# Kernel optimization log

Measured on AMD Instinct MI355X. Metric: run time of the kernel, lower is better.

The kernel has to match this reference:

```python
import jax, jax.numpy as jnp
import numpy as np

NUM_GRAPHS = 512


def setup_inputs() -> dict:
    key = jax.random.key(0)
    ks = jax.random.split(key, 12)
    N, F = 100000, 9
    E = 1600000
    x = jax.random.normal(ks[0], (N, F), dtype=jnp.float32)
    edge_index = jax.random.randint(ks[1], (2, E), 0, N, dtype=jnp.int64)
    batch = jnp.sort(jax.random.randint(ks[2], (N,), 0, NUM_GRAPHS, dtype=jnp.int64))
    def lin(k, fan_in, fan_out):
        k1, k2 = jax.random.split(k)
        bound = 1.0 / np.sqrt(fan_in)
        W = jax.random.uniform(k1, (fan_out, fan_in), jnp.float32, -bound, bound)
        b = jax.random.uniform(k2, (fan_out,), jnp.float32, -bound, bound)
        return W, b
    W1, b1 = lin(ks[3], F, 64)
    W2, b2 = lin(ks[4], 64, 128)
    W3, b3 = lin(ks[5], 128, 64)
    Wfc, bfc = lin(ks[6], 64, 11)
    return {"x": x, "edge_index": edge_index, "batch": batch,
            "W1": W1, "b1": b1, "W2": W2, "b2": b2,
            "W3": W3, "b3": b3, "Wfc": Wfc, "bfc": bfc}


def reference(x, edge_index, batch, W1, b1, W2, b2, W3, b3, Wfc, bfc):
    N = x.shape[0]
    src, dst = edge_index[0], edge_index[1]

    def gin_layer(h, W, b):
        # GINConv (eps=0): Lin((1+eps)*h_i + sum_{j->i} h_j), then relu
        agg = jax.ops.segment_sum(h[src], dst, num_segments=N)
        return jax.nn.relu((h + agg) @ W.T + b)

    h = gin_layer(x, W1, b1)   # [N, 64]
    h = gin_layer(h, W2, b2)   # [N, 128]
    h = gin_layer(h, W3, b3)   # [N, 64]

    # global_mean_pool over graph ids
    sums = jax.ops.segment_sum(h, batch, num_segments=NUM_GRAPHS)           # [G, 64]
    counts = jax.ops.segment_sum(jnp.ones((N,), h.dtype), batch,
                                 num_segments=NUM_GRAPHS)                   # [G]
    pooled = sums / jnp.maximum(counts, 1.0)[:, None]
    return pooled @ Wfc.T + bfc  # [G, num_classes]
```

## Files before the change

kernel.cpp:

```cpp
#include <hip/hip_runtime.h>
#include <hip/hip_bf16.h>


#define NBLK 256
#define CFBS 512
#define RB   128
#define NBMAX 1024
#define SCBS 1024

__device__ inline float bf2f(unsigned short u) {
    return __uint_as_float((unsigned)u << 16);
}
__device__ inline unsigned short f2bf(float f) {
    unsigned x = __float_as_uint(f);
    return (unsigned short)((x + 0x7FFFu + ((x >> 16) & 1u)) >> 16);
}
__device__ inline float lo16(unsigned u) { return __uint_as_float(u << 16); }
__device__ inline float hi16(unsigned u) { return __uint_as_float(u & 0xFFFF0000u); }


__global__ __launch_bounds__(CFBS) void count_kernel(
    const int* __restrict__ dst, int* __restrict__ cnt, int E, int NB)
{
    __shared__ int hist[NBMAX];
    int tid = threadIdx.x;
    for (int i = tid; i < NBMAX; i += CFBS) hist[i] = 0;
    __syncthreads();
    for (int e = blockIdx.x * CFBS + tid; e < E; e += NBLK * CFBS)
        atomicAdd(&hist[dst[e] >> 7], 1);
    __syncthreads();
    for (int b = tid; b < NB; b += CFBS)
        cnt[b * NBLK + blockIdx.x] = hist[b];
}

__global__ __launch_bounds__(SCBS) void scan_k1(
    const int* __restrict__ cnt, int* __restrict__ ofs,
    int* __restrict__ part, int NT)
{
    __shared__ int tmp[SCBS];
    int i = blockIdx.x * SCBS + threadIdx.x;
    int v = (i < NT) ? cnt[i] : 0;
    tmp[threadIdx.x] = v;
    __syncthreads();
    for (int off = 1; off < SCBS; off <<= 1) {
        int t = (threadIdx.x >= off) ? tmp[threadIdx.x - off] : 0;
        __syncthreads();
        tmp[threadIdx.x] += t;
        __syncthreads();
    }
    if (i < NT) ofs[i] = tmp[threadIdx.x] - v;
    if (threadIdx.x == SCBS - 1) part[blockIdx.x] = tmp[threadIdx.x];
}

__global__ __launch_bounds__(SCBS) void scan_k2(int* __restrict__ part, int B)
{
    __shared__ int tmp[SCBS];
    int v = (threadIdx.x < B) ? part[threadIdx.x] : 0;
    tmp[threadIdx.x] = v;
    __syncthreads();
    for (int off = 1; off < SCBS; off <<= 1) {
        int t = (threadIdx.x >= off) ? tmp[threadIdx.x - off] : 0;
        __syncthreads();
        tmp[threadIdx.x] += t;
        __syncthreads();
    }
    if (threadIdx.x < B) part[threadIdx.x] = tmp[threadIdx.x] - v;
}

__global__ __launch_bounds__(SCBS) void scan_k3(
    int* __restrict__ ofs, const int* __restrict__ part, int NT)
{
    int i = blockIdx.x * SCBS + threadIdx.x;
    if (i < NT) ofs[i] += part[blockIdx.x];
}

__global__ __launch_bounds__(CFBS) void fillp_kernel(
    const int* __restrict__ src, const int* __restrict__ dst,
    const int* __restrict__ ofs, int* __restrict__ pairs, int E, int NB)
{
    __shared__ int cur[NBMAX];
    int tid = threadIdx.x;
    for (int b = tid; b < NB; b += CFBS)
        cur[b] = ofs[b * NBLK + blockIdx.x];
    __syncthreads();
    for (int e = blockIdx.x * CFBS + tid; e < E; e += NBLK * CFBS) {
        int d = dst[e];
        int b = d >> 7, dl = d & 127;
        int pos = atomicAdd(&cur[b], 1);
        pairs[pos] = (dl << 20) | src[e];
    }
}

__global__ __launch_bounds__(512) void bucket_csr_kernel(
    const int* __restrict__ pairs, const int* __restrict__ ofs,
    int* __restrict__ rowstart, int* __restrict__ eidx, int N, int E, int NB)
{
    __shared__ int deg[RB], pfx[RB], cur[RB];
    int tid = threadIdx.x;
    int b = blockIdx.x, n0 = b << 7;
    int e0 = ofs[b * NBLK];
    int e1 = (b + 1 < NB) ? ofs[(b + 1) * NBLK] : E;
    if (tid < RB) deg[tid] = 0;
    __syncthreads();
    for (int e = e0 + tid; e < e1; e += 512)
        atomicAdd(&deg[pairs[e] >> 20], 1);
    __syncthreads();
    if (tid < RB) pfx[tid] = deg[tid];
    __syncthreads();
    for (int off = 1; off < RB; off <<= 1) {
        int t = (tid < RB && tid >= off) ? pfx[tid - off] : 0;
        __syncthreads();
        if (tid < RB) pfx[tid] += t;
        __syncthreads();
    }
    if (tid < RB) {
        int ex = pfx[tid] - deg[tid];
        cur[tid] = ex;
        int n = n0 + tid;
        if (n < N) rowstart[n] = e0 + ex;
    }
    if (b == NB - 1 && tid == 0) rowstart[N] = E;
    __syncthreads();
    for (int e = e0 + tid; e < e1; e += 512) {
        int p = pairs[e];
        int pos = e0 + atomicAdd(&cur[p >> 20], 1);
        eidx[pos] = p & 0xFFFFF;
    }
}


__global__ __launch_bounds__(256) void xprep_kernel(
    const float* __restrict__ x, unsigned short* __restrict__ xb, int N)
{
    int n = blockIdx.x * 256 + threadIdx.x;
    if (n >= N) return;
    unsigned short r[16];
    #pragma unroll
    for (int k = 0; k < 9; ++k) r[k] = f2bf(x[(size_t)n * 9 + k]);
    #pragma unroll
    for (int k = 9; k < 16; ++k) r[k] = 0;
    uint4 u0, u1;
    u0.x = r[0] | ((unsigned)r[1] << 16);  u0.y = r[2] | ((unsigned)r[3] << 16);
    u0.z = r[4] | ((unsigned)r[5] << 16);  u0.w = r[6] | ((unsigned)r[7] << 16);
    u1.x = r[8] | ((unsigned)r[9] << 16);  u1.y = 0; u1.z = 0; u1.w = 0;
    *(uint4*)&xb[(size_t)n * 16]     = u0;
    *(uint4*)&xb[(size_t)n * 16 + 8] = u1;
}


__global__ __launch_bounds__(256) void node1v_kernel(
    const unsigned short* __restrict__ xb, const int* __restrict__ rs,
    const int* __restrict__ eidx, const float* __restrict__ W1,
    const float* __restrict__ b1, unsigned short* __restrict__ h1, int N)
{
    __shared__ float Wl[576];
    __shared__ float bl[64];
    for (int i = threadIdx.x; i < 576; i += 256) Wl[i] = W1[i];
    if (threadIdx.x < 64) bl[threadIdx.x] = b1[threadIdx.x];
    __syncthreads();
    int wid = threadIdx.x >> 6;
    int lane = threadIdx.x & 63;
    int g  = lane >> 2;
    int d4 = lane & 3;
    int nb = blockIdx.x * 16 + wid * 4;
    if (nb >= N) return;

    int n[4], e0[4], dg[4];
    float A0[4], A1[4], A2[4], A3[4];
    #pragma unroll
    for (int i = 0; i < 4; ++i) {
        n[i] = min(nb + i, N - 1);
        e0[i] = rs[n[i]];
        dg[i] = rs[n[i] + 1] - e0[i];
        A0[i] = A1[i] = A2[i] = A3[i] = 0.f;
    }
    #pragma unroll
    for (int i = 0; i < 4; ++i) {
        if (g == 0) {
            uint2 u = *(const uint2*)&xb[(size_t)n[i] * 16 + d4 * 4];
            A0[i] += lo16(u.x); A1[i] += hi16(u.x);
            A2[i] += lo16(u.y); A3[i] += hi16(u.y);
        }
    }
    int mdeg = max(max(dg[0], dg[1]), max(dg[2], dg[3]));
    for (int w0 = 0; w0 < mdeg; w0 += 64) {
        int sidx[4], wd[4];
        #pragma unroll
        for (int i = 0; i < 4; ++i) {
            wd[i] = min(max(dg[i] - w0, 0), 64);
            sidx[i] = (lane < wd[i]) ? eidx[e0[i] + w0 + lane] : 0;
        }
        int mwd = max(max(wd[0], wd[1]), max(wd[2], wd[3]));
        for (int c = 0; c < mwd; c += 16) {
            #pragma unroll
            for (int i = 0; i < 4; ++i) {
                int idx = c + g;
                int s = __shfl(sidx[i], idx < wd[i] ? idx : 0);
                float m = (idx < wd[i]) ? 1.f : 0.f;
                uint2 u = *(const uint2*)&xb[(size_t)s * 16 + d4 * 4];
                A0[i] += m * lo16(u.x); A1[i] += m * hi16(u.x);
                A2[i] += m * lo16(u.y); A3[i] += m * hi16(u.y);
            }
        }
    }
    #pragma unroll
    for (int m = 4; m < 64; m <<= 1) {
        #pragma unroll
        for (int i = 0; i < 4; ++i) {
            A0[i] += __shfl_xor(A0[i], m); A1[i] += __shfl_xor(A1[i], m);
            A2[i] += __shfl_xor(A2[i], m); A3[i] += __shfl_xor(A3[i], m);
        }
    }
    const float* wr = &Wl[lane * 9];
    #pragma unroll
    for (int i = 0; i < 4; ++i) {
        float xv0 = __shfl(A0[i], 0), xv1 = __shfl(A1[i], 0);
        float xv2 = __shfl(A2[i], 0), xv3 = __shfl(A3[i], 0);
        float xv4 = __shfl(A0[i], 1), xv5 = __shfl(A1[i], 1);
        float xv6 = __shfl(A2[i], 1), xv7 = __shfl(A3[i], 1);
        float xv8 = __shfl(A0[i], 2);
        float s = bl[lane] + xv0 * wr[0] + xv1 * wr[1] + xv2 * wr[2]
                + xv3 * wr[3] + xv4 * wr[4] + xv5 * wr[5] + xv6 * wr[6]
                + xv7 * wr[7] + xv8 * wr[8];
        if (nb + i < N)
            h1[(size_t)(nb + i) * 64 + lane] = f2bf(fmaxf(s, 0.f));
    }
}


template<bool BIAS_RELU>
__global__ __launch_bounds__(256) void gather64v_kernel(
    const unsigned short* __restrict__ feat, const int* __restrict__ rs,
    const int* __restrict__ eidx, const float* __restrict__ bias,
    unsigned short* __restrict__ out, int N)
{
    int wid = threadIdx.x >> 6;
    int lane = threadIdx.x & 63;
    int g  = lane >> 4;
    int d4 = lane & 15;
    int nb = blockIdx.x * 16 + wid * 4;
    if (nb >= N) return;

    int n[4], e0[4], dg[4];
    float A0[4], A1[4], A2[4], A3[4];
    #pragma unroll
    for (int i = 0; i < 4; ++i) {
        n[i] = min(nb + i, N - 1);
        e0[i] = rs[n[i]];
        dg[i] = rs[n[i] + 1] - e0[i];
        A0[i] = A1[i] = A2[i] = A3[i] = 0.f;
    }
    #pragma unroll
    for (int i = 0; i < 4; ++i) {
        if (g == 0) {
            uint2 u = *(const uint2*)&feat[(size_t)n[i] * 64 + d4 * 4];
            A0[i] += lo16(u.x); A1[i] += hi16(u.x);
            A2[i] += lo16(u.y); A3[i] += hi16(u.y);
        }
    }
    int mdeg = max(max(dg[0], dg[1]), max(dg[2], dg[3]));
    for (int w0 = 0; w0 < mdeg; w0 += 64) {
        int sidx[4], wd[4];
        #pragma unroll
        for (int i = 0; i < 4; ++i) {
            wd[i] = min(max(dg[i] - w0, 0), 64);
            sidx[i] = (lane < wd[i]) ? eidx[e0[i] + w0 + lane] : 0;
        }
        int mwd = max(max(wd[0], wd[1]), max(wd[2], wd[3]));
        for (int c = 0; c < mwd; c += 16) {
            #pragma unroll
            for (int i = 0; i < 4; ++i) {
                int i0 = c + g, i1 = c + 4 + g;
                int i2 = c + 8 + g, i3 = c + 12 + g;
                int s0 = __shfl(sidx[i], i0 < wd[i] ? i0 : 0);
                int s1 = __shfl(sidx[i], i1 < wd[i] ? i1 : 0);
                int s2 = __shfl(sidx[i], i2 < wd[i] ? i2 : 0);
                int s3 = __shfl(sidx[i], i3 < wd[i] ? i3 : 0);
                float m0 = (i0 < wd[i]) ? 1.f : 0.f;
                float m1 = (i1 < wd[i]) ? 1.f : 0.f;
                float m2 = (i2 < wd[i]) ? 1.f : 0.f;
                float m3 = (i3 < wd[i]) ? 1.f : 0.f;
                uint2 u0 = *(const uint2*)&feat[(size_t)s0 * 64 + d4 * 4];
                uint2 u1 = *(const uint2*)&feat[(size_t)s1 * 64 + d4 * 4];
                uint2 u2 = *(const uint2*)&feat[(size_t)s2 * 64 + d4 * 4];
                uint2 u3 = *(const uint2*)&feat[(size_t)s3 * 64 + d4 * 4];
                A0[i] += (m0 * lo16(u0.x) + m1 * lo16(u1.x))
                       + (m2 * lo16(u2.x) + m3 * lo16(u3.x));
                A1[i] += (m0 * hi16(u0.x) + m1 * hi16(u1.x))
                       + (m2 * hi16(u2.x) + m3 * hi16(u3.x));
                A2[i] += (m0 * lo16(u0.y) + m1 * lo16(u1.y))
                       + (m2 * lo16(u2.y) + m3 * lo16(u3.y));
                A3[i] += (m0 * hi16(u0.y) + m1 * hi16(u1.y))
                       + (m2 * hi16(u2.y) + m3 * hi16(u3.y));
            }
        }
    }
    #pragma unroll
    for (int m = 16; m < 64; m <<= 1) {
        #pragma unroll
        for (int i = 0; i < 4; ++i) {
            A0[i] += __shfl_xor(A0[i], m); A1[i] += __shfl_xor(A1[i], m);
            A2[i] += __shfl_xor(A2[i], m); A3[i] += __shfl_xor(A3[i], m);
        }
    }
    float4 bv = make_float4(0.f, 0.f, 0.f, 0.f);
    if (BIAS_RELU) bv = *(const float4*)&bias[d4 * 4];
    #pragma unroll
    for (int i = 0; i < 4; ++i) {
        if (g == 0 && nb + i < N) {
            float a0 = A0[i], a1 = A1[i], a2 = A2[i], a3 = A3[i];
            if (BIAS_RELU) {
                a0 = fmaxf(a0 + bv.x, 0.f); a1 = fmaxf(a1 + bv.y, 0.f);
                a2 = fmaxf(a2 + bv.z, 0.f); a3 = fmaxf(a3 + bv.w, 0.f);
            }
            ushort4 u;
            u.x = f2bf(a0); u.y = f2bf(a1); u.z = f2bf(a2); u.w = f2bf(a3);
            *(ushort4*)&out[(size_t)(nb + i) * 64 + d4 * 4] = u;
        }
    }
}


__global__ __launch_bounds__(256) void linear23_fused_kernel(
    const unsigned short* __restrict__ A, const float* __restrict__ W2,
    const float* __restrict__ b2, const float* __restrict__ W3,
    unsigned short* __restrict__ t3, int N)
{
    using s8v = __attribute__((ext_vector_type(8))) short;
    using f4v = __attribute__((ext_vector_type(4))) float;
    __shared__ __align__(16) unsigned short Wb2[128 * 72];
    __shared__ __align__(16) unsigned short Wb3[64 * 136];
    __shared__ __align__(16) unsigned short H2[64 * 136];
    __shared__ float bl2[128];
    int tid = threadIdx.x;
    for (int i = tid; i < 128 * 64; i += 256) {
        int o = i >> 6, k = i & 63;
        Wb2[o * 72 + k] = f2bf(W2[i]);
    }
    for (int i = tid; i < 64 * 128; i += 256) {
        int o = i >> 7, k = i & 127;
        Wb3[o * 136 + k] = f2bf(W3[i]);
    }
    if (tid < 128) bl2[tid] = b2[tid];
    __syncthreads();

    int w = tid >> 6, lane = tid & 63;
    int n0 = blockIdx.x * 64 + w * 16;
    int hl = lane >> 4;
    int ll = lane & 15;

    int an = min(n0 + ll, N - 1);
    const unsigned short* arow = &A[(size_t)an * 64 + hl * 8];
    s8v a1[2];
    a1[0] = *(const s8v*)&arow[0];
    a1[1] = *(const s8v*)&arow[32];

    #pragma unroll
    for (int c = 0; c < 8; ++c) {
        f4v acc = (f4v){0.f, 0.f, 0.f, 0.f};
        const unsigned short* wrow = &Wb2[(c * 16 + ll) * 72 + hl * 8];
        acc = __builtin_amdgcn_mfma_f32_16x16x32_bf16(a1[0], *(const s8v*)&wrow[0],  acc, 0, 0, 0);
        acc = __builtin_amdgcn_mfma_f32_16x16x32_bf16(a1[1], *(const s8v*)&wrow[32], acc, 0, 0, 0);
        int col = c * 16 + ll;
        float bv = bl2[col];
        #pragma unroll
        for (int r = 0; r < 4; ++r) {
            int nrow = w * 16 + hl * 4 + r;
            H2[nrow * 136 + col] = f2bf(fmaxf(acc[r] + bv, 0.f));
        }
    }

    const unsigned short* hrow = &H2[(w * 16 + ll) * 136 + hl * 8];
    s8v a2[4];
    #pragma unroll
    for (int ks = 0; ks < 4; ++ks) a2[ks] = *(const s8v*)&hrow[ks * 32];

    #pragma unroll
    for (int c = 0; c < 4; ++c) {
        f4v acc = (f4v){0.f, 0.f, 0.f, 0.f};
        const unsigned short* wrow = &Wb3[(c * 16 + ll) * 136 + hl * 8];
        #pragma unroll
        for (int ks = 0; ks < 4; ++ks)
            acc = __builtin_amdgcn_mfma_f32_16x16x32_bf16(a2[ks], *(const s8v*)&wrow[ks * 32], acc, 0, 0, 0);
        int col = c * 16 + ll;
        #pragma unroll
        for (int r = 0; r < 4; ++r) {
            int gn = n0 + hl * 4 + r;
            if (gn < N)
                t3[(size_t)gn * 64 + col] = f2bf(acc[r]);
        }
    }
}


__device__ inline int lower_bound_i(const int* a, int n, int v) {
    int lo = 0, hi = n;
    while (lo < hi) {
        int mid = (lo + hi) >> 1;
        if (a[mid] < v) lo = mid + 1; else hi = mid;
    }
    return lo;
}

__global__ __launch_bounds__(256) void pool_fc_kernel(
    const unsigned short* __restrict__ h3, const int* __restrict__ batch,
    const float* __restrict__ Wfc, const float* __restrict__ bfc,
    float* __restrict__ out, int N)
{
    int g = blockIdx.x;
    int tid = threadIdx.x;
    int w = tid >> 6, lane = tid & 63;
    int lo = lower_bound_i(batch, N, g);
    int hi = lower_bound_i(batch, N, g + 1);
    float sum = 0.f;
    for (int i = lo + w; i < hi; i += 4)
        sum += bf2f(h3[(size_t)i * 64 + lane]);
    __shared__ float P[4][64];
    P[w][lane] = sum;
    __syncthreads();
    if (w == 0) {
        float s = P[0][lane] + P[1][lane] + P[2][lane] + P[3][lane];
        float cnt = (float)((hi - lo) > 0 ? (hi - lo) : 1);
        P[0][lane] = s / cnt;
    }
    __syncthreads();
    if (tid < 11) {
        float s = bfc[tid];
        const float* wr = &Wfc[tid * 64];
        #pragma unroll 8
        for (int k = 0; k < 64; ++k) s += P[0][k] * wr[k];
        out[g * 11 + tid] = s;
    }
}


extern "C" void kernel_launch(void* const* d_in, const int* in_sizes, int n_in,
                              void* d_out, int out_size, void* d_ws, size_t ws_size,
                              hipStream_t stream) {
    const float* x    = (const float*)d_in[0];
    const int*   ei   = (const int*)d_in[1];
    const int*   batch= (const int*)d_in[2];
    const float* W1   = (const float*)d_in[3];
    const float* b1   = (const float*)d_in[4];
    const float* W2   = (const float*)d_in[5];
    const float* b2   = (const float*)d_in[6];
    const float* W3   = (const float*)d_in[7];
    const float* b3   = (const float*)d_in[8];
    const float* Wfc  = (const float*)d_in[9];
    const float* bfc  = (const float*)d_in[10];
    float* out = (float*)d_out;

    const int N = in_sizes[2];
    const int E = in_sizes[1] / 2;
    const int G = out_size / 11;
    const int* src = ei;
    const int* dst = ei + E;
    const int NB = (N + RB - 1) / RB;
    const int NT = NB * NBLK;
    const int SB = (NT + SCBS - 1) / SCBS;

    unsigned short* B1 = (unsigned short*)d_ws;
    unsigned short* B2 = B1 + (size_t)64 * N;
    unsigned short* XB = B2 + (size_t)64 * N;
    int* pairs    = (int*)(XB + (size_t)16 * N);
    int* eidx     = pairs + E;
    int* rowstart = eidx + E;
    int* cnt      = rowstart + (N + 1);
    int* ofs      = cnt + NT;
    int* part     = ofs + NT;

    unsigned short* h1   = B1;
    unsigned short* buf2 = B2;
    unsigned short* t3   = B1;
    unsigned short* h3   = B2;
    unsigned short* xb   = XB;

    count_kernel<<<NBLK, CFBS, 0, stream>>>(dst, cnt, E, NB);
    scan_k1<<<SB, SCBS, 0, stream>>>(cnt, ofs, part, NT);
    scan_k2<<<1, SCBS, 0, stream>>>(part, SB);
    scan_k3<<<SB, SCBS, 0, stream>>>(ofs, part, NT);
    fillp_kernel<<<NBLK, CFBS, 0, stream>>>(src, dst, ofs, pairs, E, NB);
    bucket_csr_kernel<<<NB, 512, 0, stream>>>(pairs, ofs, rowstart, eidx, N, E, NB);
    xprep_kernel<<<(N + 255) / 256, 256, 0, stream>>>(x, xb, N);

    node1v_kernel<<<(N + 15) / 16, 256, 0, stream>>>(
        xb, rowstart, eidx, W1, b1, h1, N);

    gather64v_kernel<false><<<(N + 15) / 16, 256, 0, stream>>>(
        h1, rowstart, eidx, nullptr, buf2, N);
    linear23_fused_kernel<<<(N + 63) / 64, 256, 0, stream>>>(
        buf2, W2, b2, W3, t3, N);

    gather64v_kernel<true><<<(N + 15) / 16, 256, 0, stream>>>(
        t3, rowstart, eidx, b3, h3, N);

    pool_fc_kernel<<<G, 256, 0, stream>>>(h3, batch, Wfc, bfc, out, N);
}
```

Baseline: 223.2 us.

## Pre-convert W2/W3 to bf16 once and halve gather unroll width

Adds a small wprep kernel that converts W2 and W3 to bf16 once per call into workspace. The fused linear kernel then reads weight fragments straight from global memory instead of having every block convert and stage them in LDS. This removes per-block conversion work and most of the LDS footprint, which may allow more blocks per CU, but weight reads now go through cache instead of LDS. Separately, the gather loop handles 8 neighbors per step instead of 16, which lowers register pressure but leaves fewer loads in flight.

```diff
diff --git a/kernel.cpp b/kernel.cpp
--- a/kernel.cpp
+++ b/kernel.cpp
@@ -145,6 +145,15 @@
     u1.x = r[8] | ((unsigned)r[9] << 16);  u1.y = 0; u1.z = 0; u1.w = 0;
     *(uint4*)&xb[(size_t)n * 16]     = u0;
     *(uint4*)&xb[(size_t)n * 16 + 8] = u1;
+}
+
+__global__ __launch_bounds__(256) void wprep_kernel(
+    const float* __restrict__ W2, const float* __restrict__ W3,
+    unsigned short* __restrict__ w2b, unsigned short* __restrict__ w3b)
+{
+    int i = blockIdx.x * 256 + threadIdx.x;
+    if (i < 128 * 64) w2b[i] = f2bf(W2[i]);
+    if (i < 64 * 128) w3b[i] = f2bf(W3[i]);
 }
 
 
@@ -267,31 +276,20 @@
             sidx[i] = (lane < wd[i]) ? eidx[e0[i] + w0 + lane] : 0;
         }
         int mwd = max(max(wd[0], wd[1]), max(wd[2], wd[3]));
-        for (int c = 0; c < mwd; c += 16) {
+        for (int c = 0; c < mwd; c += 8) {
             #pragma unroll
             for (int i = 0; i < 4; ++i) {
                 int i0 = c + g, i1 = c + 4 + g;
-                int i2 = c + 8 + g, i3 = c + 12 + g;
                 int s0 = __shfl(sidx[i], i0 < wd[i] ? i0 : 0);
                 int s1 = __shfl(sidx[i], i1 < wd[i] ? i1 : 0);
-                int s2 = __shfl(sidx[i], i2 < wd[i] ? i2 : 0);
-                int s3 = __shfl(sidx[i], i3 < wd[i] ? i3 : 0);
                 float m0 = (i0 < wd[i]) ? 1.f : 0.f;
                 float m1 = (i1 < wd[i]) ? 1.f : 0.f;
-                float m2 = (i2 < wd[i]) ? 1.f : 0.f;
-                float m3 = (i3 < wd[i]) ? 1.f : 0.f;
                 uint2 u0 = *(const uint2*)&feat[(size_t)s0 * 64 + d4 * 4];
                 uint2 u1 = *(const uint2*)&feat[(size_t)s1 * 64 + d4 * 4];
-                uint2 u2 = *(const uint2*)&feat[(size_t)s2 * 64 + d4 * 4];
-                uint2 u3 = *(const uint2*)&feat[(size_t)s3 * 64 + d4 * 4];
-                A0[i] += (m0 * lo16(u0.x) + m1 * lo16(u1.x))
-                       + (m2 * lo16(u2.x) + m3 * lo16(u3.x));
-                A1[i] += (m0 * hi16(u0.x) + m1 * hi16(u1.x))
-                       + (m2 * hi16(u2.x) + m3 * hi16(u3.x));
-                A2[i] += (m0 * lo16(u0.y) + m1 * lo16(u1.y))
-                       + (m2 * lo16(u2.y) + m3 * lo16(u3.y));
-                A3[i] += (m0 * hi16(u0.y) + m1 * hi16(u1.y))
-                       + (m2 * hi16(u2.y) + m3 * hi16(u3.y));
+                A0[i] += m0 * lo16(u0.x) + m1 * lo16(u1.x);
+                A1[i] += m0 * hi16(u0.x) + m1 * hi16(u1.x);
+                A2[i] += m0 * lo16(u0.y) + m1 * lo16(u1.y);
+                A3[i] += m0 * hi16(u0.y) + m1 * hi16(u1.y);
             }
         }
     }
@@ -322,28 +320,14 @@
 
 
 __global__ __launch_bounds__(256) void linear23_fused_kernel(
-    const unsigned short* __restrict__ A, const float* __restrict__ W2,
-    const float* __restrict__ b2, const float* __restrict__ W3,
+    const unsigned short* __restrict__ A, const unsigned short* __restrict__ w2b,
+    const float* __restrict__ b2, const unsigned short* __restrict__ w3b,
     unsigned short* __restrict__ t3, int N)
 {
     using s8v = __attribute__((ext_vector_type(8))) short;
     using f4v = __attribute__((ext_vector_type(4))) float;
-    __shared__ __align__(16) unsigned short Wb2[128 * 72];
-    __shared__ __align__(16) unsigned short Wb3[64 * 136];
     __shared__ __align__(16) unsigned short H2[64 * 136];
-    __shared__ float bl2[128];
     int tid = threadIdx.x;
-    for (int i = tid; i < 128 * 64; i += 256) {
-        int o = i >> 6, k = i & 63;
-        Wb2[o * 72 + k] = f2bf(W2[i]);
-    }
-    for (int i = tid; i < 64 * 128; i += 256) {
-        int o = i >> 7, k = i & 127;
-        Wb3[o * 136 + k] = f2bf(W3[i]);
-    }
-    if (tid < 128) bl2[tid] = b2[tid];
-    __syncthreads();
-
     int w = tid >> 6, lane = tid & 63;
     int n0 = blockIdx.x * 64 + w * 16;
     int hl = lane >> 4;
@@ -358,11 +342,11 @@
     #pragma unroll
     for (int c = 0; c < 8; ++c) {
         f4v acc = (f4v){0.f, 0.f, 0.f, 0.f};
-        const unsigned short* wrow = &Wb2[(c * 16 + ll) * 72 + hl * 8];
+        const unsigned short* wrow = &w2b[(c * 16 + ll) * 64 + hl * 8];
         acc = __builtin_amdgcn_mfma_f32_16x16x32_bf16(a1[0], *(const s8v*)&wrow[0],  acc, 0, 0, 0);
         acc = __builtin_amdgcn_mfma_f32_16x16x32_bf16(a1[1], *(const s8v*)&wrow[32], acc, 0, 0, 0);
         int col = c * 16 + ll;
-        float bv = bl2[col];
+        float bv = b2[col];
         #pragma unroll
         for (int r = 0; r < 4; ++r) {
             int nrow = w * 16 + hl * 4 + r;
@@ -378,7 +362,7 @@
     #pragma unroll
     for (int c = 0; c < 4; ++c) {
         f4v acc = (f4v){0.f, 0.f, 0.f, 0.f};
-        const unsigned short* wrow = &Wb3[(c * 16 + ll) * 136 + hl * 8];
+        const unsigned short* wrow = &w3b[(c * 16 + ll) * 128 + hl * 8];
         #pragma unroll
         for (int ks = 0; ks < 4; ++ks)
             acc = __builtin_amdgcn_mfma_f32_16x16x32_bf16(a2[ks], *(const s8v*)&wrow[ks * 32], acc, 0, 0, 0);
@@ -468,6 +452,9 @@
     int* cnt      = rowstart + (N + 1);
     int* ofs      = cnt + NT;
     int* part     = ofs + NT;
+    unsigned short* w2b =
+        (unsigned short*)(((uintptr_t)(part + SCBS) + 15) & ~(uintptr_t)15);
+    unsigned short* w3b = w2b + 128 * 64;
 
     unsigned short* h1   = B1;
     unsigned short* buf2 = B2;
@@ -482,6 +469,7 @@
     fillp_kernel<<<NBLK, CFBS, 0, stream>>>(src, dst, ofs, pairs, E, NB);
     bucket_csr_kernel<<<NB, 512, 0, stream>>>(pairs, ofs, rowstart, eidx, N, E, NB);
     xprep_kernel<<<(N + 255) / 256, 256, 0, stream>>>(x, xb, N);
+    wprep_kernel<<<32, 256, 0, stream>>>(W2, W3, w2b, w3b);
 
     node1v_kernel<<<(N + 15) / 16, 256, 0, stream>>>(
         xb, rowstart, eidx, W1, b1, h1, N);
@@ -489,7 +477,7 @@
     gather64v_kernel<false><<<(N + 15) / 16, 256, 0, stream>>>(
         h1, rowstart, eidx, nullptr, buf2, N);
     linear23_fused_kernel<<<(N + 63) / 64, 256, 0, stream>>>(
-        buf2, W2, b2, W3, t3, N);
+        buf2, w2b, b2, w3b, t3, N);
 
     gather64v_kernel<true><<<(N + 15) / 16, 256, 0, stream>>>(
         t3, rowstart, eidx, b3, h3, N);
```

Result: no change. 224.1 us (+0.4%).
